# Kernel tuning notes

Hardware: AMD Instinct MI355X
Metric: run time of the kernel (lower is better)

The kernel has to match this reference:

```python
import jax, jax.numpy as jnp
import numpy as np

IN_DIM, D, B, N = 6, 256, 2048, 100  # inner_dim=latent_dim=256, max_size=100


def _glorot(key, shape):
    fan = sum(shape)
    return jax.random.uniform(key, shape, jnp.float32, -1.0, 1.0) * np.sqrt(6.0 / fan)


def setup_inputs() -> dict:
    key = jax.random.key(0)
    ks = jax.random.split(key, 16)
    inp = {
        "x": jax.random.normal(ks[0], (B, N, IN_DIM), jnp.float32),
        "full": 1,
        "remap_w": _glorot(ks[1], (D, IN_DIM)),
        "remap_b": jnp.zeros((D,), jnp.float32),
    }
    for l in range(4):
        k = jax.random.split(ks[2 + l], 3)
        inp[f"w{l+1}"] = _glorot(k[0], (D, D))          # GATConv lin weight (bias=False)
        inp[f"as{l+1}"] = _glorot(k[1], (D,)) * 0.1      # att_src
        inp[f"ad{l+1}"] = _glorot(k[2], (D,)) * 0.1      # att_dst
        inp[f"b{l+1}"] = jnp.zeros((D,), jnp.float32)    # post-aggregation bias
    return inp


def _gat(h, w, a_src, a_dst, b):
    # Complete digraph with self-loops (full=True path) => dense softmax attention.
    g = jnp.einsum("bnd,od->bno", h, w)                  # [B,N,D] transformed nodes
    s_src = jnp.einsum("bno,o->bn", g, a_src)            # score of node as source j
    s_dst = jnp.einsum("bno,o->bn", g, a_dst)            # score of node as target i
    logits = jax.nn.leaky_relu(s_dst[:, :, None] + s_src[:, None, :], 0.2)  # [B,i,j]
    attn = jax.nn.softmax(logits, axis=-1)               # softmax over sources per target
    return jnp.einsum("bij,bjo->bio", attn, g) + b


def reference(x, full, remap_w, remap_b,
              w1, as1, ad1, b1, w2, as2, ad2, b2,
              w3, as3, ad3, b3, w4, as4, ad4, b4):
    h = jax.nn.relu(jnp.einsum("bni,oi->bno", x, remap_w) + remap_b)
    h = jax.nn.relu(_gat(h, w1, as1, ad1, b1) + h)
    h = jax.nn.relu(_gat(h, w2, as2, ad2, b2) + h)
    h = jax.nn.relu(_gat(h, w3, as3, ad3, b3) + h)
    h = _gat(h, w4, as4, ad4, b4)
    return h
```

## Files before the change

### kernel.cpp

```cpp
#include <hip/hip_runtime.h>
#include <hip/hip_bf16.h>


typedef __attribute__((ext_vector_type(8))) short bf16x8;
typedef __attribute__((ext_vector_type(4))) short bf16x4;
typedef __attribute__((ext_vector_type(4))) float f32x4;

__device__ __forceinline__ float bf2f(unsigned short u) {
    return __uint_as_float(((unsigned)u) << 16);
}
__device__ __forceinline__ short f2bfs(float f) {
    __hip_bfloat16 h = __float2bfloat16(f);
    return *reinterpret_cast<short*>(&h);
}

#define HS_OFF 0
#define GT_OFF 51200
#define P_OFF  116736
#define SS_OFF 145408
#define SD_OFF 145856
#define SMEM_BYTES 146304

__device__ __forceinline__ int hs_addr(int row, int col) {
    return HS_OFF + row * 512 + ((col * 2) ^ ((row & 7) << 4));
}
__device__ __forceinline__ int gt_addr(int o, int n) {
    return GT_OFF + o * 256 + ((n * 2) ^ ((o & 7) << 4));
}
__device__ __forceinline__ int p_addr(int i, int j) {
    return P_OFF + i * 256 + ((j * 2) ^ ((i & 7) << 4));
}
__device__ __forceinline__ int st_addr(int row, int f) {
    return row * 1024 + ((f * 4) ^ ((row & 7) << 4));
}

struct LayerPtrs {
    const float* w[4];
    const float* bias[4];
};
struct PrepPtrs {
    const float* w[4];
    const float* as_[4];
    const float* ad_[4];
};

__global__ __launch_bounds__(256) void prep_kernel(PrepPtrs p, unsigned short* wsd) {
    const int l = blockIdx.x;
    const int d = threadIdx.x;
    __shared__ float As[256], Ad[256];
    As[d] = p.as_[l][d];
    Ad[d] = p.ad_[l][d];
    __syncthreads();
    const float* W = p.w[l];
    float s1 = 0.f, s2 = 0.f;
    for (int o = 0; o < 256; ++o) {
        float wv = W[o * 256 + d];
        s1 = fmaf(wv, As[o], s1);
        s2 = fmaf(wv, Ad[o], s2);
    }
    wsd[l * 512 + d]       = (unsigned short)f2bfs(s1);
    wsd[l * 512 + 256 + d] = (unsigned short)f2bfs(s2);
}

__global__ __launch_bounds__(256) void prep_w_kernel(PrepPtrs p, unsigned short* wbf) {
    const int l = blockIdx.x >> 4, seg = blockIdx.x & 15;
    const float* W = p.w[l];
    const int base = seg * 4096;
    for (int i = base + threadIdx.x; i < base + 4096; i += 256)
        wbf[l * 65536 + i] = (unsigned short)f2bfs(W[i]);
}

__global__ __launch_bounds__(1024) void geom_kernel(
    const float* __restrict__ x,
    const float* __restrict__ remap_w,
    const float* __restrict__ remap_b,
    LayerPtrs lp,
    const unsigned short* __restrict__ wsd,
    const unsigned short* __restrict__ wbf,
    float* __restrict__ out)
{
    extern __shared__ char smem[];
    const int tid  = threadIdx.x;
    const int lane = tid & 63;
    const int wv   = tid >> 6;
    const int c    = lane & 15;
    const int q    = lane >> 4;
    const int b    = blockIdx.x;
    const int ft   = wv;

    for (int off = tid * 16; off < 65536; off += 1024 * 16) {
        *(f32x4*)(smem + GT_OFF + off) = f32x4{0.f, 0.f, 0.f, 0.f};
    }

    {
        const int o = tid & 255, quarter = tid >> 8;
        float rw[6];
#pragma unroll
        for (int i = 0; i < 6; ++i) rw[i] = remap_w[o * 6 + i];
        const float rb = remap_b[o];
        const float* xb = x + (size_t)b * 600;
        for (int n = quarter * 25; n < quarter * 25 + 25; ++n) {
            float v = rb;
#pragma unroll
            for (int i = 0; i < 6; ++i) v = fmaf(xb[n * 6 + i], rw[i], v);
            v = fmaxf(v, 0.f);
            *(unsigned short*)(smem + hs_addr(n, o)) = (unsigned short)f2bfs(v);
        }
    }

    for (int l = 0; l < 4; ++l) {
        __syncthreads();

        {
            f32x4 acc[7];
#pragma unroll
            for (int mt = 0; mt < 7; ++mt) acc[mt] = f32x4{0.f, 0.f, 0.f, 0.f};
#pragma unroll
            for (int half = 0; half < 2; ++half) {
                bf16x8 wf[4];
                if (wbf) {
                    const unsigned short* wp =
                        wbf + l * 65536 + (ft * 16 + c) * 256 + half * 128 + q * 8;
#pragma unroll
                    for (int kk = 0; kk < 4; ++kk) wf[kk] = *(const bf16x8*)(wp + kk * 32);
                } else {
                    const float* wp = lp.w[l] + (ft * 16 + c) * 256 + half * 128 + q * 8;
#pragma unroll
                    for (int kk = 0; kk < 4; ++kk) {
                        f32x4 lo = *(const f32x4*)(wp + kk * 32);
                        f32x4 hi = *(const f32x4*)(wp + kk * 32 + 4);
                        bf16x8 w0;
#pragma unroll
                        for (int j = 0; j < 4; ++j) {
                            w0[j]     = f2bfs(lo[j]);
                            w0[4 + j] = f2bfs(hi[j]);
                        }
                        wf[kk] = w0;
                    }
                }
#pragma unroll
                for (int mt = 0; mt < 7; ++mt) {
                    int r = mt * 16 + c;
                    if (r > 99) r = 99;
#pragma unroll
                    for (int kk = 0; kk < 4; ++kk) {
                        bf16x8 af = *(const bf16x8*)(
                            smem + hs_addr(r, half * 128 + kk * 32 + q * 8));
                        acc[mt] = __builtin_amdgcn_mfma_f32_16x16x32_bf16(af, wf[kk],
                                                                          acc[mt], 0, 0, 0);
                    }
                }
            }
#pragma unroll
            for (int mt = 0; mt < 7; ++mt) {
                bf16x4 g;
#pragma unroll
                for (int j = 0; j < 4; ++j) g[j] = f2bfs(acc[mt][j]);
                *(bf16x4*)(smem + gt_addr(ft * 16 + c, mt * 16 + q * 4)) = g;
            }
        }
        if (wv >= 9) {
            const int st = wv - 9;
            int r = st * 16 + c;
            if (r > 99) r = 99;
            const unsigned short* wsp = wsd + l * 512 + q * 8;
            const unsigned short* wdp = wsp + 256;
            f32x4 sa = {0,0,0,0};
#pragma unroll
            for (int kk = 0; kk < 8; ++kk) {
                bf16x8 af = *(const bf16x8*)(smem + hs_addr(r, kk * 32 + q * 8));
                bf16x8 bs = *(const bf16x8*)(wsp + kk * 32);
                bf16x8 bd = *(const bf16x8*)(wdp + kk * 32);
                bf16x8 bz = {0,0,0,0,0,0,0,0};
                bf16x8 bb = (c == 0) ? bs : ((c == 1) ? bd : bz);
                sa = __builtin_amdgcn_mfma_f32_16x16x32_bf16(af, bb, sa, 0, 0, 0);
            }
            if (c < 2) {
                float* dst = (float*)(smem + (c == 0 ? SS_OFF : SD_OFF));
#pragma unroll
                for (int j = 0; j < 4; ++j) dst[st * 16 + q * 4 + j] = sa[j];
            }
        }
        __syncthreads();

        {
            const int i = tid >> 3, s3 = tid & 7;
            if (i < 112) {
                const float sd = ((float*)(smem + SD_OFF))[i];
                const float* Ssf = (const float*)(smem + SS_OFF);
                float vals[2][8];
                float mx = -1e30f;
#pragma unroll
                for (int t = 0; t < 2; ++t) {
                    const int blk = t * 8 + s3;
#pragma unroll
                    for (int e = 0; e < 8; ++e) {
                        const int j = blk * 8 + e;
                        float v;
                        if (j < 100) {
                            float z = sd + Ssf[j];
                            v = (z > 0.f) ? z : 0.2f * z;
                        } else {
                            v = -1e30f;
                        }
                        vals[t][e] = v;
                        mx = fmaxf(mx, v);
                    }
                }
                mx = fmaxf(mx, __shfl_xor(mx, 1, 8));
                mx = fmaxf(mx, __shfl_xor(mx, 2, 8));
                mx = fmaxf(mx, __shfl_xor(mx, 4, 8));
                float sum = 0.f;
#pragma unroll
                for (int t = 0; t < 2; ++t)
#pragma unroll
                    for (int e = 0; e < 8; ++e) {
                        float ev = __expf(vals[t][e] - mx);
                        vals[t][e] = ev;
                        sum += ev;
                    }
                sum += __shfl_xor(sum, 1, 8);
                sum += __shfl_xor(sum, 2, 8);
                sum += __shfl_xor(sum, 4, 8);
                const float inv = 1.f / sum;
#pragma unroll
                for (int t = 0; t < 2; ++t) {
                    const int blk = t * 8 + s3;
                    bf16x8 pv;
#pragma unroll
                    for (int e = 0; e < 8; ++e) pv[e] = f2bfs(vals[t][e] * inv);
                    *(bf16x8*)(smem + p_addr(i, blk * 8)) = pv;
                }
            }
        }
        __syncthreads();

        {
            const float b0 = lp.bias[l][ft * 16 + c];
            bf16x8 gf[4];
#pragma unroll
            for (int ks = 0; ks < 4; ++ks)
                gf[ks] = *(const bf16x8*)(smem + gt_addr(ft * 16 + c, ks * 32 + q * 8));

            if (l == 3) __syncthreads();

#pragma unroll
            for (int mt = 0; mt < 7; ++mt) {
                f32x4 ae = {0,0,0,0}, ao = {0,0,0,0};
#pragma unroll
                for (int ks = 0; ks < 4; ks += 2) {
                    bf16x8 pe = *(const bf16x8*)(smem + p_addr(mt * 16 + c, ks * 32 + q * 8));
                    bf16x8 po = *(const bf16x8*)(smem + p_addr(mt * 16 + c, (ks + 1) * 32 + q * 8));
                    ae = __builtin_amdgcn_mfma_f32_16x16x32_bf16(pe, gf[ks],     ae, 0, 0, 0);
                    ao = __builtin_amdgcn_mfma_f32_16x16x32_bf16(po, gf[ks + 1], ao, 0, 0, 0);
                }
                f32x4 a = ae + ao;
                const int row = mt * 16 + q * 4;
                if (l < 3) {
#pragma unroll
                    for (int j = 0; j < 4; ++j) {
                        if (row + j < 100) {
                            const int ad = hs_addr(row + j, ft * 16 + c);
                            float r = bf2f(*(unsigned short*)(smem + ad));
                            float v = fmaxf(a[j] + b0 + r, 0.f);
                            *(unsigned short*)(smem + ad) = (unsigned short)f2bfs(v);
                        }
                    }
                } else {
#pragma unroll
                    for (int j = 0; j < 4; ++j) {
                        if (row + j < 100)
                            *(float*)(smem + st_addr(row + j, ft * 16 + c)) = a[j] + b0;
                    }
                }
            }

            if (l == 3) {
                __syncthreads();
                float* ob = out + (size_t)b * 25600;
                for (int cidx = tid; cidx < 6400; cidx += 1024) {
                    const int row = cidx >> 6, fb = cidx & 63;
                    f32x4 v = *(const f32x4*)(smem + st_addr(row, fb * 4));
                    *(f32x4*)(ob + row * 256 + fb * 4) = v;
                }
            }
        }
    }
}

extern "C" void kernel_launch(void* const* d_in, const int* in_sizes, int n_in,
                              void* d_out, int out_size, void* d_ws, size_t ws_size,
                              hipStream_t stream) {
    const float* x       = (const float*)d_in[0];
    const float* remap_w = (const float*)d_in[2];
    const float* remap_b = (const float*)d_in[3];
    PrepPtrs pp;
    LayerPtrs lp;
    for (int l = 0; l < 4; ++l) {
        lp.w[l]    = pp.w[l]   = (const float*)d_in[4 + 4 * l];
        pp.as_[l]  = (const float*)d_in[5 + 4 * l];
        pp.ad_[l]  = (const float*)d_in[6 + 4 * l];
        lp.bias[l] = (const float*)d_in[7 + 4 * l];
    }
    unsigned short* wsd = (unsigned short*)d_ws;
    unsigned short* wbf = nullptr;
    if (ws_size >= (size_t)(4096 + 4 * 65536 * 2)) {
        wbf = (unsigned short*)((char*)d_ws + 4096);
    }

    prep_kernel<<<4, 256, 0, stream>>>(pp, wsd);
    if (wbf) prep_w_kernel<<<64, 256, 0, stream>>>(pp, wbf);

    (void)hipFuncSetAttribute(reinterpret_cast<const void*>(geom_kernel),
                              hipFuncAttributeMaxDynamicSharedMemorySize, SMEM_BYTES);
    geom_kernel<<<2048, 1024, SMEM_BYTES, stream>>>(x, remap_w, remap_b, lp, wsd, wbf,
                                                    (float*)d_out);
}
```

Baseline: 654.1 us.

## Widen LDS swizzles, pre-pack weights in MFMA fragment order, trim softmax rows

Widens the XOR swizzle masks on the hidden-state, transposed-G and attention-probability LDS tiles to cut bank conflicts. The bf16 weight copy is now pre-permuted into per-lane MFMA fragment order, so each wave's weight loads are contiguous and fully coalesced. Softmax now runs only on the 100 real rows, and padding rows are zero-filled. Launch bounds add a min-blocks hint of 4, which may constrain register allocation.

Result: slower. 889.8 us (+36.0%).

```diff
diff --git a/kernel.cpp b/kernel.cpp
--- a/kernel.cpp
+++ b/kernel.cpp
@@ -22,13 +22,13 @@
 #define SMEM_BYTES 146304
 
 __device__ __forceinline__ int hs_addr(int row, int col) {
-    return HS_OFF + row * 512 + ((col * 2) ^ ((row & 7) << 4));
+    return HS_OFF + row * 512 + ((col * 2) ^ ((row & 31) << 4));
 }
 __device__ __forceinline__ int gt_addr(int o, int n) {
-    return GT_OFF + o * 256 + ((n * 2) ^ ((o & 7) << 4));
+    return GT_OFF + o * 256 + ((n * 2) ^ ((o & 15) << 4));
 }
 __device__ __forceinline__ int p_addr(int i, int j) {
-    return P_OFF + i * 256 + ((j * 2) ^ ((i & 7) << 4));
+    return P_OFF + i * 256 + ((j * 2) ^ ((i & 15) << 4));
 }
 __device__ __forceinline__ int st_addr(int row, int f) {
     return row * 1024 + ((f * 4) ^ ((row & 7) << 4));
@@ -62,21 +62,28 @@
     wsd[l * 512 + 256 + d] = (unsigned short)f2bfs(s2);
 }
 
-__global__ __launch_bounds__(256) void prep_w_kernel(PrepPtrs p, unsigned short* wbf) {
-    const int l = blockIdx.x >> 4, seg = blockIdx.x & 15;
-    const float* W = p.w[l];
-    const int base = seg * 4096;
-    for (int i = base + threadIdx.x; i < base + 4096; i += 256)
-        wbf[l * 65536 + i] = (unsigned short)f2bfs(W[i]);
-}
-
-__global__ __launch_bounds__(1024) void geom_kernel(
+__global__ __launch_bounds__(64) void prep_w3_kernel(PrepPtrs p, unsigned short* wbf3) {
+    const int bid  = blockIdx.x;
+    const int l    = bid >> 7;
+    const int ft   = (bid >> 3) & 15;
+    const int half = (bid >> 2) & 1;
+    const int kk   = bid & 3;
+    const int lane = threadIdx.x;
+    const int c    = lane & 15, q = lane >> 4;
+    const float* src = p.w[l] + (ft * 16 + c) * 256 + half * 128 + kk * 32 + q * 8;
+    bf16x8 v;
+#pragma unroll
+    for (int e = 0; e < 8; ++e) v[e] = f2bfs(src[e]);
+    *(bf16x8*)(wbf3 + ((size_t)bid * 64 + lane) * 8) = v;
+}
+
+__global__ __launch_bounds__(1024, 4) void geom_kernel(
     const float* __restrict__ x,
     const float* __restrict__ remap_w,
     const float* __restrict__ remap_b,
     LayerPtrs lp,
     const unsigned short* __restrict__ wsd,
-    const unsigned short* __restrict__ wbf,
+    const unsigned short* __restrict__ wbf3,
     float* __restrict__ out)
 {
     extern __shared__ char smem[];
@@ -118,11 +125,12 @@
 #pragma unroll
             for (int half = 0; half < 2; ++half) {
                 bf16x8 wf[4];
-                if (wbf) {
+                if (wbf3) {
                     const unsigned short* wp =
-                        wbf + l * 65536 + (ft * 16 + c) * 256 + half * 128 + q * 8;
-#pragma unroll
-                    for (int kk = 0; kk < 4; ++kk) wf[kk] = *(const bf16x8*)(wp + kk * 32);
+                        wbf3 + (((size_t)((l * 16 + ft) * 2 + half) * 4 * 64) + lane) * 8;
+#pragma unroll
+                    for (int kk = 0; kk < 4; ++kk)
+                        wf[kk] = *(const bf16x8*)(wp + kk * 512);
                 } else {
                     const float* wp = lp.w[l] + (ft * 16 + c) * 256 + half * 128 + q * 8;
 #pragma unroll
@@ -185,7 +193,7 @@
 
         {
             const int i = tid >> 3, s3 = tid & 7;
-            if (i < 112) {
+            if (i < 100) {
                 const float sd = ((float*)(smem + SD_OFF))[i];
                 const float* Ssf = (const float*)(smem + SS_OFF);
                 float vals[2][8];
@@ -231,6 +239,11 @@
                     for (int e = 0; e < 8; ++e) pv[e] = f2bfs(vals[t][e] * inv);
                     *(bf16x8*)(smem + p_addr(i, blk * 8)) = pv;
                 }
+            } else if (i < 112) {
+                bf16x8 z = {0, 0, 0, 0, 0, 0, 0, 0};
+#pragma unroll
+                for (int t = 0; t < 2; ++t)
+                    *(bf16x8*)(smem + p_addr(i, (t * 8 + s3) * 8)) = z;
             }
         }
         __syncthreads();
@@ -303,16 +316,16 @@
         lp.bias[l] = (const float*)d_in[7 + 4 * l];
     }
     unsigned short* wsd = (unsigned short*)d_ws;
-    unsigned short* wbf = nullptr;
+    unsigned short* wbf3 = nullptr;
     if (ws_size >= (size_t)(4096 + 4 * 65536 * 2)) {
-        wbf = (unsigned short*)((char*)d_ws + 4096);
+        wbf3 = (unsigned short*)((char*)d_ws + 4096);
     }
 
     prep_kernel<<<4, 256, 0, stream>>>(pp, wsd);
-    if (wbf) prep_w_kernel<<<64, 256, 0, stream>>>(pp, wbf);
+    if (wbf3) prep_w3_kernel<<<512, 64, 0, stream>>>(pp, wbf3);
 
     (void)hipFuncSetAttribute(reinterpret_cast<const void*>(geom_kernel),
                               hipFuncAttributeMaxDynamicSharedMemorySize, SMEM_BYTES);
-    geom_kernel<<<2048, 1024, SMEM_BYTES, stream>>>(x, remap_w, remap_b, lp, wsd, wbf,
+    geom_kernel<<<2048, 1024, SMEM_BYTES, stream>>>(x, remap_w, remap_b, lp, wsd, wbf3,
                                                     (float*)d_out);
 }
```
